# Performance work log

Hardware: AMD Instinct MI355X
Metric: run time of the kernel (lower is better)

Reference implementation:

```python
import jax, jax.numpy as jnp
import numpy as np

N_NODES = 50000
N_EDGES = 600000
D = 128          # in = hidden = out (forced by residual adds)
HEADS = 4
HEAD_DIM = D // HEADS
EPS = 1e-5
NEG_SLOPE = 0.2  # PyG GATConv default


def setup_inputs() -> dict:
    key = jax.random.key(0)
    ks = jax.random.split(key, 12)
    s = 1.0 / np.sqrt(D)
    x = jax.random.normal(ks[0], (N_NODES, D), dtype=jnp.float32)
    edge_index = jax.random.randint(ks[1], (2, N_EDGES), 0, N_NODES, dtype=jnp.int32)
    # conv1: GATConv(D, D//heads, heads=heads)
    W1 = jax.random.normal(ks[2], (D, D), dtype=jnp.float32) * s
    a_src1 = jax.random.normal(ks[3], (HEADS, HEAD_DIM), dtype=jnp.float32) * s
    a_dst1 = jax.random.normal(ks[4], (HEADS, HEAD_DIM), dtype=jnp.float32) * s
    b1 = jnp.zeros((D,), dtype=jnp.float32)
    # conv2: GATConv(D, D, heads=1)
    W2 = jax.random.normal(ks[5], (D, D), dtype=jnp.float32) * s
    a_src2 = jax.random.normal(ks[6], (1, D), dtype=jnp.float32) * s
    a_dst2 = jax.random.normal(ks[7], (1, D), dtype=jnp.float32) * s
    b2 = jnp.zeros((D,), dtype=jnp.float32)
    # shared AddAndNorm BatchNorm1d params (same module used twice)
    bn_gamma = jnp.ones((D,), dtype=jnp.float32)
    bn_beta = jnp.zeros((D,), dtype=jnp.float32)
    return {"x": x, "edge_index": edge_index,
            "W1": W1, "a_src1": a_src1, "a_dst1": a_dst1, "b1": b1,
            "W2": W2, "a_src2": a_src2, "a_dst2": a_dst2, "b2": b2,
            "bn_gamma": bn_gamma, "bn_beta": bn_beta}


def _gat_conv(x, W, a_src, a_dst, b, src, dst, heads, head_dim):
    n = x.shape[0]
    h = (x @ W).reshape(n, heads, head_dim)                 # [N,H,C]
    e_src = jnp.einsum('nhc,hc->nh', h, a_src)              # [N,H]
    e_dst = jnp.einsum('nhc,hc->nh', h, a_dst)
    e = jax.nn.leaky_relu(e_src[src] + e_dst[dst], NEG_SLOPE)  # [E,H]
    # segment softmax over incoming edges per destination node
    m = jax.ops.segment_max(e, dst, num_segments=n)
    alpha = jnp.exp(e - m[dst])
    denom = jax.ops.segment_sum(alpha, dst, num_segments=n)
    alpha = alpha / denom[dst]
    out = jax.ops.segment_sum(alpha[:, :, None] * h[src], dst, num_segments=n)
    return out.reshape(n, heads * head_dim) + b


def _batch_norm(x, gamma, beta):
    mean = jnp.mean(x, axis=0)
    var = jnp.var(x, axis=0)
    return (x - mean) * jax.lax.rsqrt(var + EPS) * gamma + beta


def reference(x, edge_index, W1, a_src1, a_dst1, b1, W2, a_src2, a_dst2, b2,
              bn_gamma, bn_beta):
    n = x.shape[0]
    # PyG GATConv adds self loops by default
    loops = jnp.arange(n, dtype=edge_index.dtype)
    src = jnp.concatenate([edge_index[0], loops])
    dst = jnp.concatenate([edge_index[1], loops])

    res = x
    h = _gat_conv(x, W1, a_src1, a_dst1, b1, src, dst, HEADS, HEAD_DIM)
    h = _batch_norm(h + res, bn_gamma, bn_beta)   # dropout is identity (eval)
    h = jax.nn.relu(h)
    res = h
    h = _gat_conv(h, W2, a_src2, a_dst2, b2, src, dst, 1, D)
    h = _batch_norm(h + res, bn_gamma, bn_beta)
    return h
```

## Files before the change

kernel.cpp:

```cpp
#include <hip/hip_runtime.h>
#include <math.h>

#define NN 50000
#define NE 600000
#define ET (NE + NN)
#define D 128
#define EPSB 1e-5f
#define SLOPE 0.2f
#define XPITCH 136
#define SCB 196

typedef float f32x4 __attribute__((ext_vector_type(4)));
typedef short bf16x8 __attribute__((ext_vector_type(8)));

__device__ inline unsigned short bf16r(float f) {
    unsigned int u = __float_as_uint(f);
    unsigned int r = (u + 0x7fff + ((u >> 16) & 1)) >> 16;
    return (unsigned short)r;
}
__device__ inline float bflo(unsigned int u) { return __uint_as_float(u << 16); }
__device__ inline float bfhi(unsigned int u) { return __uint_as_float(u & 0xffff0000u); }
__device__ inline float lrelu(float e) { return (e > 0.f) ? e : SLOPE * e; }

__global__ void hist_kernel(const int* __restrict__ ei, int* __restrict__ deg) {
    int e = blockIdx.x * blockDim.x + threadIdx.x;
    if (e >= ET) return;
    int dst = (e < NE) ? ei[NE + e] : (e - NE);
    atomicAdd(&deg[dst], 1);
}

__global__ __launch_bounds__(256) void scan_a_kernel(const int* __restrict__ deg,
                                                     int* __restrict__ tmp,
                                                     int* __restrict__ bsum) {
    __shared__ int sm[256];
    int t = threadIdx.x;
    int idx = blockIdx.x * 256 + t;
    int v = (idx < NN) ? deg[idx] : 0;
    sm[t] = v;
    __syncthreads();
    #pragma unroll
    for (int d = 1; d < 256; d <<= 1) {
        int add = (t >= d) ? sm[t - d] : 0;
        __syncthreads();
        sm[t] += add;
        __syncthreads();
    }
    if (idx < NN) tmp[idx] = sm[t];
    if (t == 255) bsum[blockIdx.x] = sm[255];
}

__global__ __launch_bounds__(256) void scan_b_kernel(const int* __restrict__ deg,
                                                     const int* __restrict__ tmp,
                                                     const int* __restrict__ bsum,
                                                     int* __restrict__ offs,
                                                     int* __restrict__ cur) {
    __shared__ int sm[256];
    int t = threadIdx.x;
    sm[t] = (t < SCB) ? bsum[t] : 0;
    __syncthreads();
    #pragma unroll
    for (int d = 1; d < 256; d <<= 1) {
        int add = (t >= d) ? sm[t - d] : 0;
        __syncthreads();
        sm[t] += add;
        __syncthreads();
    }
    int bpre = (blockIdx.x == 0) ? 0 : sm[blockIdx.x - 1];
    int idx = blockIdx.x * 256 + t;
    if (idx < NN) {
        int excl = bpre + tmp[idx] - deg[idx];
        offs[idx] = excl;
        cur[idx] = excl;
        if (idx == NN - 1) offs[NN] = bpre + tmp[idx];
    }
}

__global__ void scatter_kernel(const int* __restrict__ ei, int* __restrict__ cur,
                               int* __restrict__ ssrc, int* __restrict__ sdst) {
    int e = blockIdx.x * blockDim.x + threadIdx.x;
    if (e >= ET) return;
    int src, dst;
    if (e < NE) { src = ei[e]; dst = ei[NE + e]; }
    else        { src = dst = e - NE; }
    int pos = atomicAdd(&cur[dst], 1);
    ssrc[pos] = src;
    sdst[pos] = dst;
}

__global__ void wconv_kernel(const float* __restrict__ W1, const float* __restrict__ W2,
                             unsigned short* __restrict__ wt1, unsigned short* __restrict__ wt2) {
    int t = blockIdx.x * blockDim.x + threadIdx.x;
    if (t >= 2 * D * D) return;
    int i = (t < D * D) ? t : t - D * D;
    int n = i >> 7, k = i & 127;
    if (t < D * D) wt1[i] = bf16r(W1[k * D + n]);
    else           wt2[i] = bf16r(W2[k * D + n]);
}

template <bool BNRELU>
__global__ __launch_bounds__(256) void gemm_mfma_kernel(const float* __restrict__ X,
                                                        const unsigned short* __restrict__ Wt,
                                                        const float* __restrict__ scsh,
                                                        unsigned short* __restrict__ Hb, int nrows) {
    __shared__ unsigned short Xl[64 * XPITCH];
    __shared__ unsigned short Wl[128 * XPITCH];
    int t = threadIdx.x;
    int row0 = blockIdx.x * 64;

    {
        int r = t >> 1, cb = (t & 1) * 64;
        const uint4* src = (const uint4*)&Wt[r * D + cb];
        uint4* dst = (uint4*)&Wl[r * XPITCH + cb];
        #pragma unroll
        for (int j = 0; j < 8; ++j) dst[j] = src[j];
    }
    {
        int r = t >> 2, cb = (t & 3) * 32;
        int gr = row0 + r; if (gr >= nrows) gr = nrows - 1;
        const float4* src = (const float4*)&X[(long)gr * D + cb];
        #pragma unroll
        for (int j = 0; j < 8; ++j) {
            float4 v = src[j];
            if (BNRELU) {
                float4 g = *(const float4*)&scsh[cb + j * 4];
                float4 s = *(const float4*)&scsh[D + cb + j * 4];
                v.x = fmaxf(fmaf(v.x, g.x, s.x), 0.f);
                v.y = fmaxf(fmaf(v.y, g.y, s.y), 0.f);
                v.z = fmaxf(fmaf(v.z, g.z, s.z), 0.f);
                v.w = fmaxf(fmaf(v.w, g.w, s.w), 0.f);
            }
            ushort4 p;
            p.x = bf16r(v.x); p.y = bf16r(v.y);
            p.z = bf16r(v.z); p.w = bf16r(v.w);
            *(ushort4*)&Xl[r * XPITCH + cb + j * 4] = p;
        }
    }
    __syncthreads();

    int wv = t >> 6, l = t & 63;
    int lr = l & 15, lg = l >> 4;
    f32x4 acc[8];
    #pragma unroll
    for (int n = 0; n < 8; ++n) acc[n] = (f32x4){0.f, 0.f, 0.f, 0.f};

    #pragma unroll
    for (int kc = 0; kc < 4; ++kc) {
        bf16x8 a = *(const bf16x8*)&Xl[(wv * 16 + lr) * XPITCH + kc * 32 + lg * 8];
        #pragma unroll
        for (int n = 0; n < 8; ++n) {
            bf16x8 b = *(const bf16x8*)&Wl[(n * 16 + lr) * XPITCH + kc * 32 + lg * 8];
            acc[n] = __builtin_amdgcn_mfma_f32_16x16x32_bf16(a, b, acc[n], 0, 0, 0);
        }
    }
    int growb = row0 + wv * 16 + lg * 4;
    #pragma unroll
    for (int n = 0; n < 8; ++n) {
        #pragma unroll
        for (int j = 0; j < 4; ++j) {
            int gr = growb + j;
            if (gr < nrows) Hb[(long)gr * D + n * 16 + lr] = bf16r(acc[n][j]);
        }
    }
}

template <int H>
__global__ void logits_kernel(const unsigned short* __restrict__ Hb,
                              const float* __restrict__ a_src,
                              const float* __restrict__ a_dst,
                              float* __restrict__ es, float* __restrict__ ed) {
    int i = blockIdx.x * blockDim.x + threadIdx.x;
    if (i >= NN * H) return;
    int n = i / H, h = i % H;
    const int CH = D / H;
    const unsigned short* hp = Hb + (long)n * D + h * CH;
    const float* as = a_src + h * CH;
    const float* ad = a_dst + h * CH;
    float s = 0.f, d = 0.f;
    for (int c = 0; c < CH; c += 8) {
        uint4 u = *(const uint4*)&hp[c];
        float4 a0 = *(const float4*)&as[c];
        float4 a1 = *(const float4*)&as[c + 4];
        float4 b0 = *(const float4*)&ad[c];
        float4 b1 = *(const float4*)&ad[c + 4];
        float f0 = bflo(u.x), f1 = bfhi(u.x), f2 = bflo(u.y), f3 = bfhi(u.y);
        float f4 = bflo(u.z), f5 = bfhi(u.z), f6 = bflo(u.w), f7 = bfhi(u.w);
        s += f0 * a0.x + f1 * a0.y + f2 * a0.z + f3 * a0.w
           + f4 * a1.x + f5 * a1.y + f6 * a1.z + f7 * a1.w;
        d += f0 * b0.x + f1 * b0.y + f2 * b0.z + f3 * b0.w
           + f4 * b1.x + f5 * b1.y + f6 * b1.z + f7 * b1.w;
    }
    es[i] = s; ed[i] = d;
}

template <int H>
__global__ void ew_kernel(const int* __restrict__ ssrc, const int* __restrict__ sdst,
                          const float* __restrict__ es, const float* __restrict__ ed,
                          float* __restrict__ wext) {
    int i = blockIdx.x * blockDim.x + threadIdx.x;
    if (i >= ET) return;
    int s = ssrc[i], dd = sdst[i];
    if (H == 4) {
        float4 a = *(const float4*)&es[s * 4];
        float4 b = *(const float4*)&ed[dd * 4];
        float4 w;
        w.x = __expf(lrelu(a.x + b.x));
        w.y = __expf(lrelu(a.y + b.y));
        w.z = __expf(lrelu(a.z + b.z));
        w.w = __expf(lrelu(a.w + b.w));
        *(float4*)&wext[i * 4] = w;
    } else {
        wext[i] = __expf(lrelu(es[s] + ed[dd]));
    }
}

template <int H, bool RECON>
__global__ __launch_bounds__(256) void agg_kernel(const unsigned short* __restrict__ Hb,
                                                  const float* __restrict__ wext,
                                                  const int* __restrict__ offs,
                                                  const int* __restrict__ ssrc,
                                                  const float* __restrict__ bias,
                                                  const float* __restrict__ resid,
                                                  const float* __restrict__ scsh,
                                                  float* __restrict__ out) {
    int wave = threadIdx.x >> 6;
    int lane = threadIdx.x & 63;
    int dst = blockIdx.x * 4 + wave;
    if (dst >= NN) return;
    int h = (H == 1) ? 0 : (lane >> 4);
    int fo = lane * 2;
    int beg = offs[dst], end = offs[dst + 1];
    float2 a0 = {0.f,0.f}, a1 = {0.f,0.f}, a2 = {0.f,0.f}, a3 = {0.f,0.f};
    float d0 = 0.f, d1 = 0.f, d2 = 0.f, d3 = 0.f;
    int idx = beg;
    for (; idx + 3 < end; idx += 4) {
        int s0 = ssrc[idx], s1 = ssrc[idx+1], s2 = ssrc[idx+2], s3 = ssrc[idx+3];
        float w0 = wext[(idx)   * H + h];
        float w1 = wext[(idx+1) * H + h];
        float w2 = wext[(idx+2) * H + h];
        float w3 = wext[(idx+3) * H + h];
        unsigned int u0 = *(const unsigned int*)&Hb[(long)s0 * D + fo];
        unsigned int u1 = *(const unsigned int*)&Hb[(long)s1 * D + fo];
        unsigned int u2 = *(const unsigned int*)&Hb[(long)s2 * D + fo];
        unsigned int u3 = *(const unsigned int*)&Hb[(long)s3 * D + fo];
        a0.x += w0 * bflo(u0); a0.y += w0 * bfhi(u0); d0 += w0;
        a1.x += w1 * bflo(u1); a1.y += w1 * bfhi(u1); d1 += w1;
        a2.x += w2 * bflo(u2); a2.y += w2 * bfhi(u2); d2 += w2;
        a3.x += w3 * bflo(u3); a3.y += w3 * bfhi(u3); d3 += w3;
    }
    for (; idx < end; ++idx) {
        int s0 = ssrc[idx];
        float w0 = wext[idx * H + h];
        unsigned int u0 = *(const unsigned int*)&Hb[(long)s0 * D + fo];
        a0.x += w0 * bflo(u0); a0.y += w0 * bfhi(u0); d0 += w0;
    }
    float dsum = (d0 + d1) + (d2 + d3);
    float accx = (a0.x + a1.x) + (a2.x + a3.x);
    float accy = (a0.y + a1.y) + (a2.y + a3.y);
    float inv = 1.0f / dsum;
    float2 rr = *(const float2*)&resid[(long)dst * D + fo];
    if (RECON) {
        float2 g = *(const float2*)&scsh[fo];
        float2 s = *(const float2*)&scsh[D + fo];
        rr.x = fmaxf(fmaf(rr.x, g.x, s.x), 0.f);
        rr.y = fmaxf(fmaf(rr.y, g.y, s.y), 0.f);
    }
    float2 o;
    o.x = accx * inv + bias[fo]     + rr.x;
    o.y = accy * inv + bias[fo + 1] + rr.y;
    *(float2*)&out[(long)dst * D + fo] = o;
}

__global__ __launch_bounds__(128) void stats_kernel(const float* __restrict__ y,
                                                    float* __restrict__ st) {
    int f = threadIdx.x;
    float s = 0.f, q = 0.f;
    for (int r = blockIdx.x; r < NN; r += gridDim.x) {
        float v = y[(long)r * D + f];
        s += v; q += v * v;
    }
    atomicAdd(&st[f], s);
    atomicAdd(&st[D + f], q);
}

__global__ void finalize_kernel(const float* __restrict__ st,
                                const float* __restrict__ gamma,
                                const float* __restrict__ beta,
                                float* __restrict__ scsh) {
    int f = threadIdx.x;
    if (f >= D) return;
    float mean = st[f] * (1.0f / NN);
    float var = st[D + f] * (1.0f / NN) - mean * mean;
    float g = gamma[f] * rsqrtf(var + EPSB);
    scsh[f] = g;
    scsh[D + f] = beta[f] - mean * g;
}

template <bool RELU>
__global__ __launch_bounds__(256) void apply_kernel(const float* __restrict__ y,
                                                    const float* __restrict__ st,
                                                    const float* __restrict__ gamma,
                                                    const float* __restrict__ beta,
                                                    float* __restrict__ out) {
    long i = (long)(blockIdx.x * blockDim.x + threadIdx.x) * 4;
    if (i >= (long)NN * D) return;
    int f = (int)(i & (D - 1));
    const float invn = 1.0f / NN;
    float4 sv = *(const float4*)&st[f];
    float4 qv = *(const float4*)&st[D + f];
    float4 gv = *(const float4*)&gamma[f];
    float4 bv = *(const float4*)&beta[f];
    float4 v = *(const float4*)&y[i];
    float4 o;
    float m, vr, g;
    m = sv.x * invn; vr = qv.x * invn - m * m; g = gv.x * rsqrtf(vr + EPSB);
    o.x = (v.x - m) * g + bv.x;
    m = sv.y * invn; vr = qv.y * invn - m * m; g = gv.y * rsqrtf(vr + EPSB);
    o.y = (v.y - m) * g + bv.y;
    m = sv.z * invn; vr = qv.z * invn - m * m; g = gv.z * rsqrtf(vr + EPSB);
    o.z = (v.z - m) * g + bv.z;
    m = sv.w * invn; vr = qv.w * invn - m * m; g = gv.w * rsqrtf(vr + EPSB);
    o.w = (v.w - m) * g + bv.w;
    if (RELU) {
        o.x = fmaxf(o.x, 0.f); o.y = fmaxf(o.y, 0.f);
        o.z = fmaxf(o.z, 0.f); o.w = fmaxf(o.w, 0.f);
    }
    *(float4*)&out[i] = o;
}

extern "C" void kernel_launch(void* const* d_in, const int* in_sizes, int n_in,
                              void* d_out, int out_size, void* d_ws, size_t ws_size,
                              hipStream_t stream) {
    const float* x      = (const float*)d_in[0];
    const int*   ei     = (const int*)  d_in[1];
    const float* W1     = (const float*)d_in[2];
    const float* a_src1 = (const float*)d_in[3];
    const float* a_dst1 = (const float*)d_in[4];
    const float* b1     = (const float*)d_in[5];
    const float* W2     = (const float*)d_in[6];
    const float* a_src2 = (const float*)d_in[7];
    const float* a_dst2 = (const float*)d_in[8];
    const float* b2     = (const float*)d_in[9];
    const float* gamma  = (const float*)d_in[10];
    const float* beta   = (const float*)d_in[11];
    float* out = (float*)d_out;

    unsigned short* Hb = (unsigned short*)d_ws;
    float* B    = (float*)d_ws + 3200000;
    float* es1  = B + 6400000;
    float* ed1  = es1 + 200000;
    float* es2  = ed1 + 200000;
    float* ed2  = es2 + 50000;
    float* st1  = ed2 + 50000;
    float* st2  = st1 + 256;
    float* scsh1= st2 + 256;
    float* wext = scsh1 + 256;
    int*   deg  = (int*)(wext + ET * 4);
    int*   offs = deg + NN;
    int*   cur  = offs + NN + 1;
    int*   ssrc = cur + NN;
    int*   sdst = ssrc + ET;
    int*   tmp  = sdst + ET;
    int*   bsum = tmp + NN;
    unsigned short* wt1 = (unsigned short*)(bsum + SCB + 4);
    unsigned short* wt2 = wt1 + D * D;

    hipMemsetAsync(deg, 0, NN * sizeof(int), stream);
    hipMemsetAsync(st1, 0, 512 * sizeof(float), stream);

    wconv_kernel<<<(2 * D * D + 255) / 256, 256, 0, stream>>>(W1, W2, wt1, wt2);
    hist_kernel<<<(ET + 255) / 256, 256, 0, stream>>>(ei, deg);
    scan_a_kernel<<<SCB, 256, 0, stream>>>(deg, tmp, bsum);
    scan_b_kernel<<<SCB, 256, 0, stream>>>(deg, tmp, bsum, offs, cur);
    scatter_kernel<<<(ET + 255) / 256, 256, 0, stream>>>(ei, cur, ssrc, sdst);

    const int GG = (NN + 63) / 64;
    const int EB = (ET + 255) / 256;
    gemm_mfma_kernel<false><<<GG, 256, 0, stream>>>(x, wt1, nullptr, Hb, NN);
    logits_kernel<4><<<(NN * 4 + 255) / 256, 256, 0, stream>>>(Hb, a_src1, a_dst1, es1, ed1);
    ew_kernel<4><<<EB, 256, 0, stream>>>(ssrc, sdst, es1, ed1, wext);
    agg_kernel<4, false><<<(NN + 3) / 4, 256, 0, stream>>>(Hb, wext, offs, ssrc, b1, x, nullptr, B);
    stats_kernel<<<1024, 128, 0, stream>>>(B, st1);
    finalize_kernel<<<1, 128, 0, stream>>>(st1, gamma, beta, scsh1);

    gemm_mfma_kernel<true><<<GG, 256, 0, stream>>>(B, wt2, scsh1, Hb, NN);
    logits_kernel<1><<<(NN + 255) / 256, 256, 0, stream>>>(Hb, a_src2, a_dst2, es2, ed2);
    ew_kernel<1><<<EB, 256, 0, stream>>>(ssrc, sdst, es2, ed2, wext);
    agg_kernel<1, true><<<(NN + 3) / 4, 256, 0, stream>>>(Hb, wext, offs, ssrc, b2, B, scsh1, out);
    stats_kernel<<<1024, 128, 0, stream>>>(out, st2);
    apply_kernel<false><<<(NN * D / 4 + 255) / 256, 256, 0, stream>>>(out, st2, gamma, beta, out);
}
```

Measured before the change: 383.5 us.

## Fuse edge-weight computation into aggregation and store CSR sources as 16-bit

Removes the separate ew kernels and the wext buffer. Each aggregation wave now computes exp(leaky_relu(es[src]+ed[dst])) for a chunk of edges in parallel across lanes, then broadcasts weights and source ids with shuffles. The scatter no longer writes sdst, and it stores source indices as unsigned short, which is valid only because the node count fits in 16 bits. This cuts two launches and the edge-weight write/read traffic. The cost is a lower inner-loop unroll and extra shuffle work inside aggregation.

```diff
diff --git a/kernel.cpp b/kernel.cpp
--- a/kernel.cpp
+++ b/kernel.cpp
@@ -76,15 +76,14 @@
 }
 
 __global__ void scatter_kernel(const int* __restrict__ ei, int* __restrict__ cur,
-                               int* __restrict__ ssrc, int* __restrict__ sdst) {
+                               unsigned short* __restrict__ ssrc) {
     int e = blockIdx.x * blockDim.x + threadIdx.x;
     if (e >= ET) return;
     int src, dst;
     if (e < NE) { src = ei[e]; dst = ei[NE + e]; }
     else        { src = dst = e - NE; }
     int pos = atomicAdd(&cur[dst], 1);
-    ssrc[pos] = src;
-    sdst[pos] = dst;
+    ssrc[pos] = (unsigned short)src;
 }
 
 __global__ void wconv_kernel(const float* __restrict__ W1, const float* __restrict__ W2,
@@ -192,70 +191,61 @@
     es[i] = s; ed[i] = d;
 }
 
-template <int H>
-__global__ void ew_kernel(const int* __restrict__ ssrc, const int* __restrict__ sdst,
-                          const float* __restrict__ es, const float* __restrict__ ed,
-                          float* __restrict__ wext) {
-    int i = blockIdx.x * blockDim.x + threadIdx.x;
-    if (i >= ET) return;
-    int s = ssrc[i], dd = sdst[i];
-    if (H == 4) {
-        float4 a = *(const float4*)&es[s * 4];
-        float4 b = *(const float4*)&ed[dd * 4];
-        float4 w;
-        w.x = __expf(lrelu(a.x + b.x));
-        w.y = __expf(lrelu(a.y + b.y));
-        w.z = __expf(lrelu(a.z + b.z));
-        w.w = __expf(lrelu(a.w + b.w));
-        *(float4*)&wext[i * 4] = w;
-    } else {
-        wext[i] = __expf(lrelu(es[s] + ed[dd]));
-    }
-}
-
 template <int H, bool RECON>
 __global__ __launch_bounds__(256) void agg_kernel(const unsigned short* __restrict__ Hb,
-                                                  const float* __restrict__ wext,
+                                                  const float* __restrict__ es,
+                                                  const float* __restrict__ ed,
                                                   const int* __restrict__ offs,
-                                                  const int* __restrict__ ssrc,
+                                                  const unsigned short* __restrict__ ssrc,
                                                   const float* __restrict__ bias,
                                                   const float* __restrict__ resid,
                                                   const float* __restrict__ scsh,
                                                   float* __restrict__ out) {
+    const int CHK = 64 / H;
     int wave = threadIdx.x >> 6;
     int lane = threadIdx.x & 63;
     int dst = blockIdx.x * 4 + wave;
     if (dst >= NN) return;
-    int h = (H == 1) ? 0 : (lane >> 4);
+    int h  = (H == 1) ? 0 : (lane >> 4);
+    int hh = lane & (H - 1);
     int fo = lane * 2;
     int beg = offs[dst], end = offs[dst + 1];
-    float2 a0 = {0.f,0.f}, a1 = {0.f,0.f}, a2 = {0.f,0.f}, a3 = {0.f,0.f};
-    float d0 = 0.f, d1 = 0.f, d2 = 0.f, d3 = 0.f;
-    int idx = beg;
-    for (; idx + 3 < end; idx += 4) {
-        int s0 = ssrc[idx], s1 = ssrc[idx+1], s2 = ssrc[idx+2], s3 = ssrc[idx+3];
-        float w0 = wext[(idx)   * H + h];
-        float w1 = wext[(idx+1) * H + h];
-        float w2 = wext[(idx+2) * H + h];
-        float w3 = wext[(idx+3) * H + h];
-        unsigned int u0 = *(const unsigned int*)&Hb[(long)s0 * D + fo];
-        unsigned int u1 = *(const unsigned int*)&Hb[(long)s1 * D + fo];
-        unsigned int u2 = *(const unsigned int*)&Hb[(long)s2 * D + fo];
-        unsigned int u3 = *(const unsigned int*)&Hb[(long)s3 * D + fo];
-        a0.x += w0 * bflo(u0); a0.y += w0 * bfhi(u0); d0 += w0;
-        a1.x += w1 * bflo(u1); a1.y += w1 * bfhi(u1); d1 += w1;
-        a2.x += w2 * bflo(u2); a2.y += w2 * bfhi(u2); d2 += w2;
-        a3.x += w3 * bflo(u3); a3.y += w3 * bfhi(u3); d3 += w3;
-    }
-    for (; idx < end; ++idx) {
-        int s0 = ssrc[idx];
-        float w0 = wext[idx * H + h];
-        unsigned int u0 = *(const unsigned int*)&Hb[(long)s0 * D + fo];
-        a0.x += w0 * bflo(u0); a0.y += w0 * bfhi(u0); d0 += w0;
-    }
-    float dsum = (d0 + d1) + (d2 + d3);
-    float accx = (a0.x + a1.x) + (a2.x + a3.x);
-    float accy = (a0.y + a1.y) + (a2.y + a3.y);
+    int cnt = end - beg;
+    float edv = ed[dst * H + hh];
+
+    float ax0 = 0.f, ay0 = 0.f, ax1 = 0.f, ay1 = 0.f;
+    float ds0 = 0.f, ds1 = 0.f;
+
+    for (int base = 0; base < cnt; base += CHK) {
+        int j = lane / H;
+        float w = 0.f;
+        int msrc = 0;
+        if (base + j < cnt) {
+            msrc = ssrc[beg + base + j];
+            w = __expf(lrelu(es[msrc * H + hh] + edv));
+        }
+        int lim = min(CHK, cnt - base);
+        int jj = 0;
+        for (; jj + 1 < lim; jj += 2) {
+            float w0 = __shfl(w, jj * H + h);
+            float w1 = __shfl(w, (jj + 1) * H + h);
+            int s0 = __shfl(msrc, jj * H);
+            int s1 = __shfl(msrc, (jj + 1) * H);
+            unsigned int u0 = *(const unsigned int*)&Hb[(long)s0 * D + fo];
+            unsigned int u1 = *(const unsigned int*)&Hb[(long)s1 * D + fo];
+            ax0 += w0 * bflo(u0); ay0 += w0 * bfhi(u0); ds0 += w0;
+            ax1 += w1 * bflo(u1); ay1 += w1 * bfhi(u1); ds1 += w1;
+        }
+        if (jj < lim) {
+            float w0 = __shfl(w, jj * H + h);
+            int s0 = __shfl(msrc, jj * H);
+            unsigned int u0 = *(const unsigned int*)&Hb[(long)s0 * D + fo];
+            ax0 += w0 * bflo(u0); ay0 += w0 * bfhi(u0); ds0 += w0;
+        }
+    }
+    float dsum = ds0 + ds1;
+    float accx = ax0 + ax1;
+    float accy = ay0 + ay1;
     float inv = 1.0f / dsum;
     float2 rr = *(const float2*)&resid[(long)dst * D + fo];
     if (RECON) {
@@ -353,16 +343,14 @@
     float* st1  = ed2 + 50000;
     float* st2  = st1 + 256;
     float* scsh1= st2 + 256;
-    float* wext = scsh1 + 256;
-    int*   deg  = (int*)(wext + ET * 4);
+    int*   deg  = (int*)(scsh1 + 256);
     int*   offs = deg + NN;
     int*   cur  = offs + NN + 1;
-    int*   ssrc = cur + NN;
-    int*   sdst = ssrc + ET;
-    int*   tmp  = sdst + ET;
+    int*   tmp  = cur + NN;
     int*   bsum = tmp + NN;
-    unsigned short* wt1 = (unsigned short*)(bsum + SCB + 4);
-    unsigned short* wt2 = wt1 + D * D;
+    unsigned short* ssrc = (unsigned short*)(bsum + SCB + 4);
+    unsigned short* wt1  = ssrc + ((ET + 7) & ~7);
+    unsigned short* wt2  = wt1 + D * D;
 
     hipMemsetAsync(deg, 0, NN * sizeof(int), stream);
     hipMemsetAsync(st1, 0, 512 * sizeof(float), stream);
@@ -371,21 +359,18 @@
     hist_kernel<<<(ET + 255) / 256, 256, 0, stream>>>(ei, deg);
     scan_a_kernel<<<SCB, 256, 0, stream>>>(deg, tmp, bsum);
     scan_b_kernel<<<SCB, 256, 0, stream>>>(deg, tmp, bsum, offs, cur);
-    scatter_kernel<<<(ET + 255) / 256, 256, 0, stream>>>(ei, cur, ssrc, sdst);
+    scatter_kernel<<<(ET + 255) / 256, 256, 0, stream>>>(ei, cur, ssrc);
 
     const int GG = (NN + 63) / 64;
-    const int EB = (ET + 255) / 256;
     gemm_mfma_kernel<false><<<GG, 256, 0, stream>>>(x, wt1, nullptr, Hb, NN);
     logits_kernel<4><<<(NN * 4 + 255) / 256, 256, 0, stream>>>(Hb, a_src1, a_dst1, es1, ed1);
-    ew_kernel<4><<<EB, 256, 0, stream>>>(ssrc, sdst, es1, ed1, wext);
-    agg_kernel<4, false><<<(NN + 3) / 4, 256, 0, stream>>>(Hb, wext, offs, ssrc, b1, x, nullptr, B);
+    agg_kernel<4, false><<<(NN + 3) / 4, 256, 0, stream>>>(Hb, es1, ed1, offs, ssrc, b1, x, nullptr, B);
     stats_kernel<<<1024, 128, 0, stream>>>(B, st1);
     finalize_kernel<<<1, 128, 0, stream>>>(st1, gamma, beta, scsh1);
 
     gemm_mfma_kernel<true><<<GG, 256, 0, stream>>>(B, wt2, scsh1, Hb, NN);
     logits_kernel<1><<<(NN + 255) / 256, 256, 0, stream>>>(Hb, a_src2, a_dst2, es2, ed2);
-    ew_kernel<1><<<EB, 256, 0, stream>>>(ssrc, sdst, es2, ed2, wext);
-    agg_kernel<1, true><<<(NN + 3) / 4, 256, 0, stream>>>(Hb, wext, offs, ssrc, b2, B, scsh1, out);
+    agg_kernel<1, true><<<(NN + 3) / 4, 256, 0, stream>>>(Hb, es2, ed2, offs, ssrc, b2, B, scsh1, out);
     stats_kernel<<<1024, 128, 0, stream>>>(out, st2);
     apply_kernel<false><<<(NN * D / 4 + 255) / 256, 256, 0, stream>>>(out, st2, gamma, beta, out);
 }
```

Result: faster. 369.8 us (-3.6%).
